# Kernel tuning notes

Hardware: AMD Instinct MI355X
Metric: run time of the kernel (lower is better)

Reference implementation:

```python
import jax, jax.numpy as jnp
import numpy as np

B, T, N, E = 4, 30, 2000, 32000
F_IN, F_HID, F_GRU, N_CLS = 8, 64, 128, 2


def setup_inputs() -> dict:
    key = jax.random.key(0)
    ks = jax.random.split(key, 12)
    return {
        "x": jax.random.normal(ks[0], (B, T, N, F_IN), jnp.float32),
        "edge_index": jax.random.randint(ks[1], (B, T, 2, E), 0, N, jnp.int32),
        "W1": jax.random.normal(ks[2], (F_IN, F_HID), jnp.float32) * 0.1,
        "b1": jax.random.normal(ks[3], (F_HID,), jnp.float32) * 0.1,
        "W2": jax.random.normal(ks[4], (F_HID, F_HID), jnp.float32) * 0.1,
        "b2": jax.random.normal(ks[5], (F_HID,), jnp.float32) * 0.1,
        "W_ih": jax.random.normal(ks[6], (3 * F_GRU, F_HID), jnp.float32) * 0.1,
        "W_hh": jax.random.normal(ks[7], (3 * F_GRU, F_GRU), jnp.float32) * 0.1,
        "b_ih": jax.random.normal(ks[8], (3 * F_GRU,), jnp.float32) * 0.1,
        "b_hh": jax.random.normal(ks[9], (3 * F_GRU,), jnp.float32) * 0.1,
        "fc_w": jax.random.normal(ks[10], (N_CLS, F_GRU), jnp.float32) * 0.1,
        "fc_b": jax.random.normal(ks[11], (N_CLS,), jnp.float32) * 0.1,
    }


def _gcn_conv(x, src, dst, W, b):
    # PyG GCNConv (edge_weight=None): add self-loops, sym-normalize, x@W, scatter-add, +bias
    n = x.shape[0]
    loops = jnp.arange(n, dtype=src.dtype)
    s = jnp.concatenate([src, loops])
    d = jnp.concatenate([dst, loops])
    deg = jax.ops.segment_sum(jnp.ones(s.shape[0], x.dtype), d, num_segments=n)
    dis = jnp.where(deg > 0, jax.lax.rsqrt(deg), 0.0)
    norm = dis[s] * dis[d]                      # [E+N]
    h = x @ W                                   # [N, Fout]
    msg = h[s] * norm[:, None]                  # gather + scale
    return jax.ops.segment_sum(msg, d, num_segments=n) + b


def _frame_embed(x, ei, W1, b1, W2, b2):
    # one graph frame -> mean-pooled 64-d embedding
    src, dst = ei[0], ei[1]
    h = jax.nn.relu(_gcn_conv(x, src, dst, W1, b1))
    h = jax.nn.relu(_gcn_conv(h, src, dst, W2, b2))
    return h.mean(axis=0)


def _gru(H, W_ih, W_hh, b_ih, b_hh):
    # H: [T, B, F_HID]; torch GRU gate order: r, z, n
    def step(h, x_t):
        gi = x_t @ W_ih.T + b_ih                # [B, 3H]
        gh = h @ W_hh.T + b_hh
        i_r, i_z, i_n = jnp.split(gi, 3, axis=-1)
        h_r, h_z, h_n = jnp.split(gh, 3, axis=-1)
        r = jax.nn.sigmoid(i_r + h_r)
        z = jax.nn.sigmoid(i_z + h_z)
        n = jnp.tanh(i_n + r * h_n)
        h_new = (1.0 - z) * n + z * h
        return h_new, None
    h0 = jnp.zeros((H.shape[1], F_GRU), H.dtype)
    h_final, _ = jax.lax.scan(step, h0, H)
    return h_final                              # [B, F_GRU]


def reference(x, edge_index, W1, b1, W2, b2, W_ih, W_hh, b_ih, b_hh, fc_w, fc_b):
    G = B * T
    xf = x.reshape(G, N, F_IN)
    eif = edge_index.reshape(G, 2, E)
    emb = jax.vmap(_frame_embed, in_axes=(0, 0, None, None, None, None))(
        xf, eif, W1, b1, W2, b2)                # [G, 64]
    H = emb.reshape(B, T, F_HID).transpose(1, 0, 2)  # [T, B, 64]
    h_final = _gru(H, W_ih, W_hh, b_ih, b_hh)   # [B, 128]
    return h_final @ fc_w.T + fc_b              # [B, 2]
```

## Files before the change

### kernel.cpp

```cpp
#include <hip/hip_runtime.h>
#include <math.h>

#define G    120
#define Nn   2000
#define Ee   32000
#define Tt   30
#define Bb   4
#define Fg   128
#define QCAP 9216
#define TSLOT 48

static __device__ __forceinline__ unsigned short f2bf(float f) {
    unsigned u = __float_as_uint(f);
    u += 0x7fffu + ((u >> 16) & 1u);
    return (unsigned short)(u >> 16);
}

#if defined(__has_builtin)
#if __has_builtin(__builtin_amdgcn_cvt_f32_fp8) && __has_builtin(__builtin_amdgcn_cvt_pk_fp8_f32)
#define HW_FP8 1
#endif
#if __has_builtin(__builtin_amdgcn_cvt_pk_f32_fp8)
#define HW_FP8_PK 1
typedef float floatx2 __attribute__((ext_vector_type(2)));
#endif
#endif

static __device__ __forceinline__ unsigned fp8_enc_sw(float x) {
    unsigned s = (__float_as_uint(x) >> 24) & 0x80u;
    float ax = fminf(fabsf(x), 448.f);
    unsigned em;
    if (ax < 0.015625f) {
        em = (unsigned)__float2int_rn(ax * 512.f);
    } else {
        int e = (int)(__float_as_uint(ax) >> 23) - 127;
        float r = ax * __uint_as_float((unsigned)((130 - e) << 23));
        int q = __float2int_rn(r);
        em = (unsigned)(((e + 7) << 3) + (q - 8));
        em = min(em, 126u);
    }
    return s | em;
}
static __device__ __forceinline__ float fp8_dec_sw(unsigned b) {
    unsigned em = b & 0x7fu;
    float mag;
    if (em < 8u) mag = (float)em * 0.001953125f;
    else mag = __uint_as_float((((em >> 3) + 120u) << 23) | ((em & 7u) << 20));
    return (b & 0x80u) ? -mag : mag;
}
static __device__ __forceinline__ unsigned fp8_pack4(float a, float b, float c, float d) {
#ifdef HW_FP8
    int w = __builtin_amdgcn_cvt_pk_fp8_f32(a, b, 0, false);
    w = __builtin_amdgcn_cvt_pk_fp8_f32(c, d, w, true);
    return (unsigned)w;
#else
    return fp8_enc_sw(a) | (fp8_enc_sw(b) << 8) | (fp8_enc_sw(c) << 16) | (fp8_enc_sw(d) << 24);
#endif
}
static __device__ __forceinline__ void fp8x4_dec(unsigned dw, float* o) {
#ifdef HW_FP8_PK
    floatx2 lo = __builtin_amdgcn_cvt_pk_f32_fp8((int)dw, false);
    floatx2 hi = __builtin_amdgcn_cvt_pk_f32_fp8((int)dw, true);
    o[0] = lo[0]; o[1] = lo[1]; o[2] = hi[0]; o[3] = hi[1];
#else
    o[0] = fp8_dec_sw(dw & 0xffu);
    o[1] = fp8_dec_sw((dw >> 8) & 0xffu);
    o[2] = fp8_dec_sw((dw >> 16) & 0xffu);
    o[3] = fp8_dec_sw((dw >> 24) & 0xffu);
#endif
}

__global__ void __launch_bounds__(1024, 1)
k_build(const int* __restrict__ ei, float* __restrict__ dis,
        int* __restrict__ startA, int* __restrict__ cntA,
        int* __restrict__ csr, unsigned* __restrict__ ellT,
        int* __restrict__ cntS, int* __restrict__ ordS,
        float* __restrict__ emb) {
    __shared__ int   hist[Nn];
    __shared__ float disl[Nn];
    __shared__ int   ws[512];
    __shared__ int   csr_l[QCAP];
    __shared__ int   cntQ[500];
    __shared__ int   exQ[500];
    __shared__ int   nodeAt[500];
    __shared__ int   dh[64];
    __shared__ int   db[64];
    __shared__ int   ovfS;
    int i = blockIdx.x;
    int xcd = i & 7;
    int j = i >> 3;
    int f15 = j >> 2;
    int q = j & 3;
    int g = xcd * 15 + f15;
    int gq = g * 4 + q;
    int lo = q * 500;
    int tid = threadIdx.x;
    for (int idx = tid; idx < Nn; idx += 1024) hist[idx] = 0;
    if (tid < 64) dh[tid] = 0;
    if (tid == 0) ovfS = 0;
    if (q == 0 && tid < 64) emb[g * 64 + tid] = 0.f;
    __syncthreads();
    const int* srcp = ei + (size_t)g * 2 * Ee;
    const int* dstp = srcp + Ee;
    for (int it = tid; it < Ee / 4; it += 1024) {
        int4 d = reinterpret_cast<const int4*>(dstp)[it];
        atomicAdd(&hist[d.x], 1);
        atomicAdd(&hist[d.y], 1);
        atomicAdd(&hist[d.z], 1);
        atomicAdd(&hist[d.w], 1);
    }
    __syncthreads();
    for (int idx = tid; idx < Nn; idx += 1024) disl[idx] = rsqrtf((float)hist[idx] + 1.0f);
    int cnt = 0;
    if (tid < 512) ws[tid] = (tid < 500) ? hist[lo + tid] : 0;
    if (tid < 500) cnt = hist[lo + tid];
    __syncthreads();
    for (int off = 1; off < 512; off <<= 1) {
        int v = 0;
        if (tid < 512 && tid >= off) v = ws[tid - off];
        __syncthreads();
        if (tid < 512) ws[tid] += v;
        __syncthreads();
    }
    int ex = 0;
    if (tid < 500) ex = ws[tid] - cnt;
    if (tid < 500) {
        hist[lo + tid] = ex;
        cntQ[tid] = cnt;
        exQ[tid] = ex;
        if (cnt > TSLOT - 1) atomicMax(&ovfS, 1);
        atomicAdd(&dh[min(cnt, 63)], 1);
    }
    __syncthreads();
    if (tid == 0) {
        int s = 0;
        for (int b = 0; b < 64; ++b) { db[b] = s; s += dh[b]; }
    }
    __syncthreads();
    if (tid < 64) dh[tid] = db[tid];
    __syncthreads();
    if (tid < 500) {
        int p = atomicAdd(&dh[min(cnt, 63)], 1);
        nodeAt[p] = tid;
    }
    for (int it = tid; it < Ee / 4; it += 1024) {
        int4 d = reinterpret_cast<const int4*>(dstp)[it];
        int4 s = reinterpret_cast<const int4*>(srcp)[it];
        if (d.x >= lo && d.x < lo + 500) { int p = atomicAdd(&hist[d.x], 1); if (p < QCAP) csr_l[p] = s.x; }
        if (d.y >= lo && d.y < lo + 500) { int p = atomicAdd(&hist[d.y], 1); if (p < QCAP) csr_l[p] = s.y; }
        if (d.z >= lo && d.z < lo + 500) { int p = atomicAdd(&hist[d.z], 1); if (p < QCAP) csr_l[p] = s.z; }
        if (d.w >= lo && d.w < lo + 500) { int p = atomicAdd(&hist[d.w], 1); if (p < QCAP) csr_l[p] = s.w; }
    }
    __syncthreads();
    if (tid < 500) {
        int n_own = lo + tid;
        size_t gn_own = (size_t)g * Nn + n_own;
        cntA[gn_own] = cnt;
        startA[gn_own] = gq * QCAP + ex;
        dis[gn_own] = disl[n_own];
        int sl = nodeAt[tid];
        int n2 = lo + sl;
        int cnt2 = cntQ[sl];
        int ex2 = exQ[sl];
        int c = q * 500 + tid;
        size_t gc = (size_t)g * Nn + c;
        cntS[gc] = cnt2;
        ordS[gc] = n2;
        float dn2 = disl[n2];
        unsigned* et = ellT + (size_t)g * TSLOT * Nn + c;
        et[0] = (unsigned)n2 | ((unsigned)f2bf(dn2 * dn2) << 16);
        int m2 = min(cnt2, TSLOT - 1);
        for (int e = 0; e < m2; ++e) {
            int s = csr_l[ex2 + e];
            et[(size_t)(e + 1) * Nn] = (unsigned)s | ((unsigned)f2bf(disl[s] * dn2) << 16);
        }
    }
    __syncthreads();
    if (ovfS) {
        int total = ws[511];
        int* cg = csr + (size_t)gq * QCAP;
        for (int it = tid; it < total; it += 1024) cg[it] = csr_l[it];
    }
}

__global__ void __launch_bounds__(256)
k_fused(const float* __restrict__ x, const unsigned* __restrict__ ellT,
        const int* __restrict__ cntS, const int* __restrict__ ordS,
        const int* __restrict__ startA, const int* __restrict__ csr,
        const float* __restrict__ dis,
        const float* __restrict__ W1, const float* __restrict__ b1,
        const float* __restrict__ W2, unsigned char* __restrict__ t2f) {
    int i = blockIdx.x;
    int xcd = i & 7;
    int j = i >> 3;
    int g = xcd * 15 + (j >> 3);
    int blk = j & 7;
    int p = blk * 256 + threadIdx.x;
    bool valid = (p < Nn);
    size_t gp = (size_t)g * Nn + (valid ? p : 0);
    int n = valid ? ordS[gp] : 0;
    int cnt = valid ? cntS[gp] : 0;
    int myc = valid ? (min(cnt, TSLOT - 1) + 1) : 0;
    float aX[8];
#pragma unroll
    for (int k = 0; k < 8; ++k) aX[k] = 0.f;
    {
        const unsigned* et = ellT + (size_t)g * TSLOT * Nn + (valid ? p : 0);
        const float4* x4 = reinterpret_cast<const float4*>(x + (size_t)g * Nn * 8);
        for (int e0 = 0; e0 < TSLOT; e0 += 8) {
            if (!__any(e0 < myc)) break;
            unsigned ub[8];
#pragma unroll
            for (int k = 0; k < 8; ++k)
                ub[k] = (e0 + k < myc) ? et[(size_t)(e0 + k) * Nn] : 0u;
#pragma unroll
            for (int k = 0; k < 8; ++k) {
                if (e0 + k < myc) {
                    float w = __uint_as_float(ub[k] & 0xffff0000u);
                    int s = ub[k] & 0xffffu;
                    float4 r0 = x4[s * 2], r1 = x4[s * 2 + 1];
                    aX[0] += r0.x * w; aX[1] += r0.y * w; aX[2] += r0.z * w; aX[3] += r0.w * w;
                    aX[4] += r1.x * w; aX[5] += r1.y * w; aX[6] += r1.z * w; aX[7] += r1.w * w;
                }
            }
        }
        if (cnt > TSLOT - 1) {
            size_t gn = (size_t)g * Nn + n;
            float dn = dis[gn];
            int start = startA[gn];
            const float* dsg = dis + (size_t)g * Nn;
            for (int e = TSLOT - 1; e < cnt; ++e) {
                int s = csr[start + e];
                float w = dsg[s] * dn;
                float4 r0 = x4[s * 2], r1 = x4[s * 2 + 1];
                aX[0] += r0.x * w; aX[1] += r0.y * w; aX[2] += r0.z * w; aX[3] += r0.w * w;
                aX[4] += r1.x * w; aX[5] += r1.y * w; aX[6] += r1.z * w; aX[7] += r1.w * w;
            }
        }
    }
    float h1r[64];
    {
        const float4* b14 = reinterpret_cast<const float4*>(b1);
#pragma unroll
        for (int f4 = 0; f4 < 16; ++f4) {
            float4 b = b14[f4];
            h1r[4 * f4 + 0] = b.x; h1r[4 * f4 + 1] = b.y;
            h1r[4 * f4 + 2] = b.z; h1r[4 * f4 + 3] = b.w;
        }
        const float4* W14 = reinterpret_cast<const float4*>(W1);
#pragma unroll
        for (int k = 0; k < 8; ++k) {
            float hk = aX[k];
#pragma unroll
            for (int f4 = 0; f4 < 16; ++f4) {
                float4 w = W14[k * 16 + f4];
                h1r[4 * f4 + 0] += hk * w.x; h1r[4 * f4 + 1] += hk * w.y;
                h1r[4 * f4 + 2] += hk * w.z; h1r[4 * f4 + 3] += hk * w.w;
            }
        }
#pragma unroll
        for (int f = 0; f < 64; ++f) h1r[f] = fmaxf(h1r[f], 0.f);
    }
    uint4 oh[2][2];
    {
        const float4* W24 = reinterpret_cast<const float4*>(W2);
#pragma unroll
        for (int hf = 0; hf < 2; ++hf) {
            float acch[32];
#pragma unroll
            for (int f = 0; f < 32; ++f) acch[f] = 0.f;
#pragma unroll
            for (int k = 0; k < 64; ++k) {
                float hk = h1r[k];
#pragma unroll
                for (int f4 = 0; f4 < 8; ++f4) {
                    float4 w = W24[k * 16 + hf * 8 + f4];
                    acch[4 * f4 + 0] += hk * w.x; acch[4 * f4 + 1] += hk * w.y;
                    acch[4 * f4 + 2] += hk * w.z; acch[4 * f4 + 3] += hk * w.w;
                }
            }
            oh[hf][0].x = fp8_pack4(acch[0],  acch[1],  acch[2],  acch[3]);
            oh[hf][0].y = fp8_pack4(acch[4],  acch[5],  acch[6],  acch[7]);
            oh[hf][0].z = fp8_pack4(acch[8],  acch[9],  acch[10], acch[11]);
            oh[hf][0].w = fp8_pack4(acch[12], acch[13], acch[14], acch[15]);
            oh[hf][1].x = fp8_pack4(acch[16], acch[17], acch[18], acch[19]);
            oh[hf][1].y = fp8_pack4(acch[20], acch[21], acch[22], acch[23]);
            oh[hf][1].z = fp8_pack4(acch[24], acch[25], acch[26], acch[27]);
            oh[hf][1].w = fp8_pack4(acch[28], acch[29], acch[30], acch[31]);
        }
    }
    if (valid) {
        uint4* op = reinterpret_cast<uint4*>(t2f + ((size_t)g * Nn + n) * 64);
        op[0] = oh[0][0]; op[1] = oh[0][1]; op[2] = oh[1][0]; op[3] = oh[1][1];
    }
}

__global__ void __launch_bounds__(1024, 1)
k_aggF(const unsigned char* __restrict__ t2f, const unsigned* __restrict__ ellT,
       const int* __restrict__ cntS, const int* __restrict__ ordS,
       const int* __restrict__ startA, const int* __restrict__ csr,
       const float* __restrict__ dis, const float* __restrict__ bias,
       float* __restrict__ emb) {
    __shared__ uint4 stage[Nn * 5];
    int i = blockIdx.x;
    int xcd = i & 7;
    int j = i >> 3;
    int g = xcd * 15 + (j >> 1);
    int half = j & 1;
    int tid = threadIdx.x;
    int w = tid >> 6, lane = tid & 63;
    {
        const uint4* src = reinterpret_cast<const uint4*>(t2f + (size_t)g * Nn * 64);
        for (int it = tid; it < Nn * 4; it += 1024)
            stage[(it >> 2) * 5 + (it & 3)] = src[it];
    }
    __syncthreads();
#define ROWFMA(dw, base) { float o_[4]; fp8x4_dec(dw, o_); \
    acc[base + 0] += o_[0] * wt; acc[base + 1] += o_[1] * wt; \
    acc[base + 2] += o_[2] * wt; acc[base + 3] += o_[3] * wt; }
    int po = w * 64 + lane;
    int p = half * 1000 + po;
    bool valid = (po < 1000);
    size_t gp = (size_t)g * Nn + (valid ? p : 0);
    int cnt = valid ? cntS[gp] : 0;
    int myc = valid ? (min(cnt, TSLOT - 1) + 1) : 0;
    float acc[64];
#pragma unroll
    for (int k = 0; k < 64; ++k) acc[k] = 0.f;
    const unsigned* et = ellT + (size_t)g * TSLOT * Nn + (valid ? p : 0);
    for (int e = 0; e < TSLOT; ++e) {
        if (!__any(e < myc)) break;
        if (e < myc) {
            unsigned u = et[(size_t)e * Nn];
            float wt = __uint_as_float(u & 0xffff0000u);
            int s = u & 0xffffu;
            uint4 r0 = stage[s * 5], r1 = stage[s * 5 + 1];
            uint4 r2 = stage[s * 5 + 2], r3 = stage[s * 5 + 3];
            ROWFMA(r0.x, 0)  ROWFMA(r0.y, 4)  ROWFMA(r0.z, 8)  ROWFMA(r0.w, 12)
            ROWFMA(r1.x, 16) ROWFMA(r1.y, 20) ROWFMA(r1.z, 24) ROWFMA(r1.w, 28)
            ROWFMA(r2.x, 32) ROWFMA(r2.y, 36) ROWFMA(r2.z, 40) ROWFMA(r2.w, 44)
            ROWFMA(r3.x, 48) ROWFMA(r3.y, 52) ROWFMA(r3.z, 56) ROWFMA(r3.w, 60)
        }
    }
    if (cnt > TSLOT - 1) {
        int n = ordS[gp];
        size_t gn = (size_t)g * Nn + n;
        float dn = dis[gn];
        int start = startA[gn];
        const float* dsg = dis + (size_t)g * Nn;
        for (int e = TSLOT - 1; e < cnt; ++e) {
            int s = csr[start + e];
            float wt = dsg[s] * dn;
            uint4 r0 = stage[s * 5], r1 = stage[s * 5 + 1];
            uint4 r2 = stage[s * 5 + 2], r3 = stage[s * 5 + 3];
            ROWFMA(r0.x, 0)  ROWFMA(r0.y, 4)  ROWFMA(r0.z, 8)  ROWFMA(r0.w, 12)
            ROWFMA(r1.x, 16) ROWFMA(r1.y, 20) ROWFMA(r1.z, 24) ROWFMA(r1.w, 28)
            ROWFMA(r2.x, 32) ROWFMA(r2.y, 36) ROWFMA(r2.z, 40) ROWFMA(r2.w, 44)
            ROWFMA(r3.x, 48) ROWFMA(r3.y, 52) ROWFMA(r3.z, 56) ROWFMA(r3.w, 60)
        }
    }
#undef ROWFMA
    float pool = 0.f;
#pragma unroll
    for (int k = 0; k < 64; ++k) {
        float v = valid ? fmaxf(acc[k] + bias[k], 0.f) : 0.f;
        v += __shfl_xor(v, 1);  v += __shfl_xor(v, 2);  v += __shfl_xor(v, 4);
        v += __shfl_xor(v, 8);  v += __shfl_xor(v, 16); v += __shfl_xor(v, 32);
        if (lane == k) pool = v;
    }
    atomicAdd(&emb[g * 64 + lane], pool * (1.0f / Nn));
}

__global__ void __launch_bounds__(768, 1)
k_gru_seq(const float* __restrict__ emb, const float* __restrict__ W_ih,
          const float* __restrict__ b_ih, const float* __restrict__ W_hh,
          const float* __restrict__ b_hh, const float* __restrict__ fc_w,
          const float* __restrict__ fc_b, float* __restrict__ out) {
    __shared__ float h[Fg];
    __shared__ float part[768];
    __shared__ float embs[Tt][64];
    __shared__ float pgi[Tt][768];
    int b = blockIdx.x;
    int tid = threadIdx.x;
    int row = tid >> 1;
    int half = tid & 1;
    float w[64];
    const float* wr = W_hh + (size_t)row * Fg + half * 64;
#pragma unroll
    for (int i = 0; i < 64; ++i) w[i] = wr[i];
    float wih[32];
    const float* wir = W_ih + (size_t)row * 64 + half * 32;
#pragma unroll
    for (int i = 0; i < 32; ++i) wih[i] = wir[i];
    for (int it = tid; it < Tt * 64; it += 768)
        embs[it >> 6][it & 63] = emb[((size_t)b * Tt) * 64 + it];
    if (tid < Fg) h[tid] = 0.f;
    __syncthreads();
    for (int t = 0; t < Tt; ++t) {
        const float* e = &embs[t][half * 32];
        float a0 = 0.f, a1 = 0.f, a2 = 0.f, a3 = 0.f;
#pragma unroll
        for (int i = 0; i < 8; ++i) {
            a0 += wih[4 * i + 0] * e[4 * i + 0];
            a1 += wih[4 * i + 1] * e[4 * i + 1];
            a2 += wih[4 * i + 2] * e[4 * i + 2];
            a3 += wih[4 * i + 3] * e[4 * i + 3];
        }
        pgi[t][tid] = (a0 + a1) + (a2 + a3);
    }
    __syncthreads();
    for (int t = 0; t < Tt; ++t) {
        const float* hh = &h[half * 64];
        float a0 = 0.f, a1 = 0.f, a2 = 0.f, a3 = 0.f;
#pragma unroll
        for (int i = 0; i < 16; ++i) {
            a0 += w[4 * i + 0] * hh[4 * i + 0];
            a1 += w[4 * i + 1] * hh[4 * i + 1];
            a2 += w[4 * i + 2] * hh[4 * i + 2];
            a3 += w[4 * i + 3] * hh[4 * i + 3];
        }
        part[tid] = (a0 + a1) + (a2 + a3);
        __syncthreads();
        if (tid < Fg) {
            int j = tid;
            float hr = b_hh[j]       + part[2 * j]           + part[2 * j + 1];
            float hz = b_hh[128 + j] + part[2 * (128 + j)]   + part[2 * (128 + j) + 1];
            float hn = b_hh[256 + j] + part[2 * (256 + j)]   + part[2 * (256 + j) + 1];
            float gr = b_ih[j]       + pgi[t][2 * j]         + pgi[t][2 * j + 1];
            float gz = b_ih[128 + j] + pgi[t][2 * (128 + j)] + pgi[t][2 * (128 + j) + 1];
            float gn = b_ih[256 + j] + pgi[t][2 * (256 + j)] + pgi[t][2 * (256 + j) + 1];
            float r  = 1.f / (1.f + expf(-(gr + hr)));
            float z  = 1.f / (1.f + expf(-(gz + hz)));
            float nn = tanhf(gn + r * hn);
            h[j] = (1.f - z) * nn + z * h[j];
        }
        __syncthreads();
    }
    if (tid < 2) {
        float acc = fc_b[tid];
        for (int k = 0; k < Fg; ++k) acc += fc_w[tid * Fg + k] * h[k];
        out[b * 2 + tid] = acc;
    }
}

extern "C" void kernel_launch(void* const* d_in, const int* in_sizes, int n_in,
                              void* d_out, int out_size, void* d_ws, size_t ws_size,
                              hipStream_t stream) {
    const float* x     = (const float*)d_in[0];
    const int*   ei    = (const int*)  d_in[1];
    const float* W1    = (const float*)d_in[2];
    const float* b1    = (const float*)d_in[3];
    const float* W2    = (const float*)d_in[4];
    const float* b2    = (const float*)d_in[5];
    const float* W_ih  = (const float*)d_in[6];
    const float* W_hh  = (const float*)d_in[7];
    const float* b_ih  = (const float*)d_in[8];
    const float* b_hh  = (const float*)d_in[9];
    const float* fc_w  = (const float*)d_in[10];
    const float* fc_b  = (const float*)d_in[11];
    float* out = (float*)d_out;

    char* ws = (char*)d_ws;
    size_t off = 0;
    auto alloc = [&](size_t bytes) -> void* {
        void* p = ws + off;
        off = (off + bytes + 255) & ~(size_t)255;
        return p;
    };
    float*    dis    = (float*)   alloc((size_t)G * Nn * 4);
    int*      startA = (int*)     alloc((size_t)G * Nn * 4);
    int*      cntA   = (int*)     alloc((size_t)G * Nn * 4);
    int*      cntS   = (int*)     alloc((size_t)G * Nn * 4);
    int*      ordS   = (int*)     alloc((size_t)G * Nn * 4);
    int*      csr    = (int*)     alloc((size_t)G * 4 * QCAP * 4);
    unsigned* ellT   = (unsigned*)alloc((size_t)G * TSLOT * Nn * 4);
    unsigned char* t2f = (unsigned char*)alloc((size_t)G * Nn * 64);
    float*    emb    = (float*)   alloc((size_t)G * 64 * 4);
    (void)ws_size; (void)in_sizes; (void)n_in; (void)out_size;

    hipLaunchKernelGGL(k_build,   dim3(480), dim3(1024), 0, stream, ei, dis, startA, cntA, csr, ellT, cntS, ordS, emb);
    hipLaunchKernelGGL(k_fused,   dim3(960), dim3(256), 0, stream, x, ellT, cntS, ordS, startA, csr, dis, W1, b1, W2, t2f);
    hipLaunchKernelGGL(k_aggF,    dim3(240), dim3(1024), 0, stream, t2f, ellT, cntS, ordS, startA, csr, dis, b2, emb);
    hipLaunchKernelGGL(k_gru_seq, dim3(Bb), dim3(768), 0, stream, emb, W_ih, b_ih, W_hh, b_hh, fc_w, fc_b, out);
}
```

Before: 260.5 us.

## Split degree histogram into separate kernel and prefetch ELL entries in aggregation

Adds a k_deg kernel that computes the full-graph in-degree histogram and dis once per frame. Before, each of the four quarter-blocks in k_build repeated that full histogram. k_build now loads dis, histograms only the destinations in its own quarter, and drops the unused cntA output. The aggregation loop in k_aggF software-prefetches the next ELL entry so its global load overlaps the current edge's FMA work. The cost is an extra kernel launch plus a global round trip for dis.

```diff
diff --git a/kernel.cpp b/kernel.cpp
--- a/kernel.cpp
+++ b/kernel.cpp
@@ -71,12 +71,32 @@
 }
 
 __global__ void __launch_bounds__(1024, 1)
-k_build(const int* __restrict__ ei, float* __restrict__ dis,
-        int* __restrict__ startA, int* __restrict__ cntA,
-        int* __restrict__ csr, unsigned* __restrict__ ellT,
-        int* __restrict__ cntS, int* __restrict__ ordS,
-        float* __restrict__ emb) {
-    __shared__ int   hist[Nn];
+k_deg(const int* __restrict__ ei, float* __restrict__ dis, float* __restrict__ emb) {
+    __shared__ int hist[Nn];
+    int g = blockIdx.x;
+    int tid = threadIdx.x;
+    for (int idx = tid; idx < Nn; idx += 1024) hist[idx] = 0;
+    if (tid < 64) emb[g * 64 + tid] = 0.f;
+    __syncthreads();
+    const int* dstp = ei + (size_t)g * 2 * Ee + Ee;
+    for (int it = tid; it < Ee / 4; it += 1024) {
+        int4 d = reinterpret_cast<const int4*>(dstp)[it];
+        atomicAdd(&hist[d.x], 1);
+        atomicAdd(&hist[d.y], 1);
+        atomicAdd(&hist[d.z], 1);
+        atomicAdd(&hist[d.w], 1);
+    }
+    __syncthreads();
+    for (int idx = tid; idx < Nn; idx += 1024)
+        dis[(size_t)g * Nn + idx] = rsqrtf((float)hist[idx] + 1.0f);
+}
+
+__global__ void __launch_bounds__(1024, 1)
+k_build(const int* __restrict__ ei, const float* __restrict__ dis,
+        int* __restrict__ startA, int* __restrict__ csr,
+        unsigned* __restrict__ ellT, int* __restrict__ cntS,
+        int* __restrict__ ordS) {
+    __shared__ int   histq[500];
     __shared__ float disl[Nn];
     __shared__ int   ws[512];
     __shared__ int   csr_l[QCAP];
@@ -95,25 +115,24 @@
     int gq = g * 4 + q;
     int lo = q * 500;
     int tid = threadIdx.x;
-    for (int idx = tid; idx < Nn; idx += 1024) hist[idx] = 0;
+    for (int idx = tid; idx < Nn; idx += 1024) disl[idx] = dis[(size_t)g * Nn + idx];
+    if (tid < 500) histq[tid] = 0;
     if (tid < 64) dh[tid] = 0;
     if (tid == 0) ovfS = 0;
-    if (q == 0 && tid < 64) emb[g * 64 + tid] = 0.f;
     __syncthreads();
     const int* srcp = ei + (size_t)g * 2 * Ee;
     const int* dstp = srcp + Ee;
     for (int it = tid; it < Ee / 4; it += 1024) {
         int4 d = reinterpret_cast<const int4*>(dstp)[it];
-        atomicAdd(&hist[d.x], 1);
-        atomicAdd(&hist[d.y], 1);
-        atomicAdd(&hist[d.z], 1);
-        atomicAdd(&hist[d.w], 1);
-    }
-    __syncthreads();
-    for (int idx = tid; idx < Nn; idx += 1024) disl[idx] = rsqrtf((float)hist[idx] + 1.0f);
+        if ((unsigned)(d.x - lo) < 500u) atomicAdd(&histq[d.x - lo], 1);
+        if ((unsigned)(d.y - lo) < 500u) atomicAdd(&histq[d.y - lo], 1);
+        if ((unsigned)(d.z - lo) < 500u) atomicAdd(&histq[d.z - lo], 1);
+        if ((unsigned)(d.w - lo) < 500u) atomicAdd(&histq[d.w - lo], 1);
+    }
+    __syncthreads();
     int cnt = 0;
-    if (tid < 512) ws[tid] = (tid < 500) ? hist[lo + tid] : 0;
-    if (tid < 500) cnt = hist[lo + tid];
+    if (tid < 512) ws[tid] = (tid < 500) ? histq[tid] : 0;
+    if (tid < 500) cnt = histq[tid];
     __syncthreads();
     for (int off = 1; off < 512; off <<= 1) {
         int v = 0;
@@ -125,7 +144,7 @@
     int ex = 0;
     if (tid < 500) ex = ws[tid] - cnt;
     if (tid < 500) {
-        hist[lo + tid] = ex;
+        histq[tid] = ex;
         cntQ[tid] = cnt;
         exQ[tid] = ex;
         if (cnt > TSLOT - 1) atomicMax(&ovfS, 1);
@@ -146,18 +165,16 @@
     for (int it = tid; it < Ee / 4; it += 1024) {
         int4 d = reinterpret_cast<const int4*>(dstp)[it];
         int4 s = reinterpret_cast<const int4*>(srcp)[it];
-        if (d.x >= lo && d.x < lo + 500) { int p = atomicAdd(&hist[d.x], 1); if (p < QCAP) csr_l[p] = s.x; }
-        if (d.y >= lo && d.y < lo + 500) { int p = atomicAdd(&hist[d.y], 1); if (p < QCAP) csr_l[p] = s.y; }
-        if (d.z >= lo && d.z < lo + 500) { int p = atomicAdd(&hist[d.z], 1); if (p < QCAP) csr_l[p] = s.z; }
-        if (d.w >= lo && d.w < lo + 500) { int p = atomicAdd(&hist[d.w], 1); if (p < QCAP) csr_l[p] = s.w; }
+        if ((unsigned)(d.x - lo) < 500u) { int p = atomicAdd(&histq[d.x - lo], 1); if (p < QCAP) csr_l[p] = s.x; }
+        if ((unsigned)(d.y - lo) < 500u) { int p = atomicAdd(&histq[d.y - lo], 1); if (p < QCAP) csr_l[p] = s.y; }
+        if ((unsigned)(d.z - lo) < 500u) { int p = atomicAdd(&histq[d.z - lo], 1); if (p < QCAP) csr_l[p] = s.z; }
+        if ((unsigned)(d.w - lo) < 500u) { int p = atomicAdd(&histq[d.w - lo], 1); if (p < QCAP) csr_l[p] = s.w; }
     }
     __syncthreads();
     if (tid < 500) {
         int n_own = lo + tid;
         size_t gn_own = (size_t)g * Nn + n_own;
-        cntA[gn_own] = cnt;
         startA[gn_own] = gq * QCAP + ex;
-        dis[gn_own] = disl[n_own];
         int sl = nodeAt[tid];
         int n2 = lo + sl;
         int cnt2 = cntQ[sl];
@@ -318,6 +335,13 @@
 #define ROWFMA(dw, base) { float o_[4]; fp8x4_dec(dw, o_); \
     acc[base + 0] += o_[0] * wt; acc[base + 1] += o_[1] * wt; \
     acc[base + 2] += o_[2] * wt; acc[base + 3] += o_[3] * wt; }
+#define EDGEFMA(s, wt) { \
+    uint4 r0 = stage[(s) * 5], r1 = stage[(s) * 5 + 1]; \
+    uint4 r2 = stage[(s) * 5 + 2], r3 = stage[(s) * 5 + 3]; \
+    ROWFMA(r0.x, 0)  ROWFMA(r0.y, 4)  ROWFMA(r0.z, 8)  ROWFMA(r0.w, 12) \
+    ROWFMA(r1.x, 16) ROWFMA(r1.y, 20) ROWFMA(r1.z, 24) ROWFMA(r1.w, 28) \
+    ROWFMA(r2.x, 32) ROWFMA(r2.y, 36) ROWFMA(r2.z, 40) ROWFMA(r2.w, 44) \
+    ROWFMA(r3.x, 48) ROWFMA(r3.y, 52) ROWFMA(r3.z, 56) ROWFMA(r3.w, 60) }
     int po = w * 64 + lane;
     int p = half * 1000 + po;
     bool valid = (po < 1000);
@@ -328,19 +352,17 @@
 #pragma unroll
     for (int k = 0; k < 64; ++k) acc[k] = 0.f;
     const unsigned* et = ellT + (size_t)g * TSLOT * Nn + (valid ? p : 0);
+    unsigned u_cur = (0 < myc) ? et[0] : 0u;
     for (int e = 0; e < TSLOT; ++e) {
         if (!__any(e < myc)) break;
+        unsigned u_nxt = ((e + 1) < TSLOT && (e + 1) < myc)
+                             ? et[(size_t)(e + 1) * Nn] : 0u;
         if (e < myc) {
-            unsigned u = et[(size_t)e * Nn];
-            float wt = __uint_as_float(u & 0xffff0000u);
-            int s = u & 0xffffu;
-            uint4 r0 = stage[s * 5], r1 = stage[s * 5 + 1];
-            uint4 r2 = stage[s * 5 + 2], r3 = stage[s * 5 + 3];
-            ROWFMA(r0.x, 0)  ROWFMA(r0.y, 4)  ROWFMA(r0.z, 8)  ROWFMA(r0.w, 12)
-            ROWFMA(r1.x, 16) ROWFMA(r1.y, 20) ROWFMA(r1.z, 24) ROWFMA(r1.w, 28)
-            ROWFMA(r2.x, 32) ROWFMA(r2.y, 36) ROWFMA(r2.z, 40) ROWFMA(r2.w, 44)
-            ROWFMA(r3.x, 48) ROWFMA(r3.y, 52) ROWFMA(r3.z, 56) ROWFMA(r3.w, 60)
-        }
+            float wt = __uint_as_float(u_cur & 0xffff0000u);
+            int s = u_cur & 0xffffu;
+            EDGEFMA(s, wt)
+        }
+        u_cur = u_nxt;
     }
     if (cnt > TSLOT - 1) {
         int n = ordS[gp];
@@ -351,14 +373,10 @@
         for (int e = TSLOT - 1; e < cnt; ++e) {
             int s = csr[start + e];
             float wt = dsg[s] * dn;
-            uint4 r0 = stage[s * 5], r1 = stage[s * 5 + 1];
-            uint4 r2 = stage[s * 5 + 2], r3 = stage[s * 5 + 3];
-            ROWFMA(r0.x, 0)  ROWFMA(r0.y, 4)  ROWFMA(r0.z, 8)  ROWFMA(r0.w, 12)
-            ROWFMA(r1.x, 16) ROWFMA(r1.y, 20) ROWFMA(r1.z, 24) ROWFMA(r1.w, 28)
-            ROWFMA(r2.x, 32) ROWFMA(r2.y, 36) ROWFMA(r2.z, 40) ROWFMA(r2.w, 44)
-            ROWFMA(r3.x, 48) ROWFMA(r3.y, 52) ROWFMA(r3.z, 56) ROWFMA(r3.w, 60)
-        }
-    }
+            EDGEFMA(s, wt)
+        }
+    }
+#undef EDGEFMA
 #undef ROWFMA
     float pool = 0.f;
 #pragma unroll
@@ -469,7 +487,6 @@
     };
     float*    dis    = (float*)   alloc((size_t)G * Nn * 4);
     int*      startA = (int*)     alloc((size_t)G * Nn * 4);
-    int*      cntA   = (int*)     alloc((size_t)G * Nn * 4);
     int*      cntS   = (int*)     alloc((size_t)G * Nn * 4);
     int*      ordS   = (int*)     alloc((size_t)G * Nn * 4);
     int*      csr    = (int*)     alloc((size_t)G * 4 * QCAP * 4);
@@ -478,7 +495,8 @@
     float*    emb    = (float*)   alloc((size_t)G * 64 * 4);
     (void)ws_size; (void)in_sizes; (void)n_in; (void)out_size;
 
-    hipLaunchKernelGGL(k_build,   dim3(480), dim3(1024), 0, stream, ei, dis, startA, cntA, csr, ellT, cntS, ordS, emb);
+    hipLaunchKernelGGL(k_deg,     dim3(G), dim3(1024), 0, stream, ei, dis, emb);
+    hipLaunchKernelGGL(k_build,   dim3(480), dim3(1024), 0, stream, ei, dis, startA, csr, ellT, cntS, ordS);
     hipLaunchKernelGGL(k_fused,   dim3(960), dim3(256), 0, stream, x, ellT, cntS, ordS, startA, csr, dis, W1, b1, W2, t2f);
     hipLaunchKernelGGL(k_aggF,    dim3(240), dim3(1024), 0, stream, t2f, ellT, cntS, ordS, startA, csr, dis, b2, emb);
     hipLaunchKernelGGL(k_gru_seq, dim3(Bb), dim3(768), 0, stream, emb, W_ih, b_ih, W_hh, b_hh, fc_w, fc_b, out);
```

Result: slower. 267.4 us (+2.7%).
